# Optimization experiments

Measured on AMD Instinct MI355X. Metric: run time of the kernel, lower is better.

The kernel has to match this reference:

```python
import jax, jax.numpy as jnp
import numpy as np

EMBED_DIM = 128
NUM_EMB = 2048
COMMIT_COST = 0.25
SOFTMAX_COST = 0.0


def setup_inputs() -> dict:
    key = jax.random.key(0)
    k1, k2 = jax.random.split(key)
    z = jax.random.normal(k1, (32, EMBED_DIM, 32, 32), dtype=jnp.float32)
    limit = float(np.sqrt(3.0 / NUM_EMB))  # sonnet-style uniform init
    codebook = jax.random.uniform(k2, (NUM_EMB, EMBED_DIM), minval=-limit, maxval=limit, dtype=jnp.float32)
    return {"z": z, "codebook": codebook}


def _vq_forward(z, codebook):
    B, C, H, W = z.shape  # C == EMBED_DIM (channel_split == 1)
    sg = jax.lax.stop_gradient
    zf = jnp.moveaxis(z, 1, -1).reshape(-1, C)  # [N, d], N = B*H*W
    # squared distances: ||z||^2 + ||e||^2 - 2 z e^T  -> [N, K]
    dist = (jnp.sum(zf * zf, axis=1, keepdims=True)
            + jnp.sum(codebook * codebook, axis=1)
            - 2.0 * (zf @ codebook.T))
    # softmax histogram over spatial positions per batch element: [B, K]
    softmax_hist = jax.nn.softmax(-dist, axis=-1).reshape(B, -1, NUM_EMB).sum(axis=1)
    idx = jnp.argmin(dist, axis=1)  # [N]
    # cross entropy with logits = -dist, target = argmin index
    log_probs = jax.nn.log_softmax(-dist, axis=-1)
    softmax_loss = -jnp.mean(jnp.take_along_axis(log_probs, idx[:, None], axis=1))
    onehot = jax.nn.one_hot(idx, NUM_EMB, dtype=jnp.float32)  # [N, K]
    # index histogram (torch.histc with bins=K,min=0,max=K-1 == integer counts here)
    index_hist = onehot.reshape(B, -1, NUM_EMB).sum(axis=1)  # [B, K]
    zq = (onehot @ codebook).reshape(B, H, W, C)
    zq = jnp.moveaxis(zq, -1, 1)  # [B, C, H, W]
    commitment_loss = jnp.mean((sg(zq) - z) ** 2)
    quantization_loss = jnp.mean((zq - sg(z)) ** 2)
    loss = quantization_loss + COMMIT_COST * commitment_loss + SOFTMAX_COST * softmax_loss
    avg_probs = onehot.mean(axis=0)
    perplexity = jnp.exp(-jnp.sum(avg_probs * jnp.log(avg_probs + 1e-10)))
    onehot_img = jnp.moveaxis(onehot.reshape(B, H, W, NUM_EMB), -1, 1)  # [B, K, H, W]
    idx_img = idx.reshape(B, 1, H, W)
    zq_ste = z + sg(zq - z)  # straight-through estimator
    return (loss, zq_ste, sg(perplexity), onehot_img, idx_img, index_hist,
            softmax_hist, sg(commitment_loss), sg(quantization_loss), sg(softmax_loss))


def reference(z, codebook):
    return _vq_forward(z, codebook)
```

## Files before the change

kernel.cpp:

```cpp
#include <hip/hip_runtime.h>
#include <hip/hip_bf16.h>
#include <float.h>


#define K_NUM 2048
#define D_NUM 128
#define B_NUM 32
#define HW_NUM 1024
#define N_NUM 32768
#define REF_EPS 0.01f

typedef __attribute__((ext_vector_type(8))) short bf16x8;
typedef __attribute__((ext_vector_type(4))) float f32x4;

#define O_LOSS   0ull
#define O_ZQ     1ull
#define O_PERP   4194305ull
#define O_ONEHOT 4194306ull
#define O_IDX    71303170ull
#define O_IHIST  71335938ull
#define O_SHIST  71401474ull
#define O_COMMIT 71467010ull
#define O_QUANT  71467011ull
#define O_SM     71467012ull

#define WS_IDX    0ull
#define WS_SCAL   131072ull
#define WS_EB     131328ull
#define WS_CNORM  1179904ull
#define WS_HIST   1188096ull
#define WS_END    17965312ull

__device__ __noinline__ float vq_exact_dist(const float* zrow, const float* erow,
                                            float zncn) {
    float dot = 0.f;
    for (int c = 0; c < 128; c += 4) {
        float4 zz = *reinterpret_cast<const float4*>(zrow + c);
        float4 ee = *reinterpret_cast<const float4*>(erow + c);
        dot = fmaf(zz.x, -2.f * ee.x, dot);
        dot = fmaf(zz.y, -2.f * ee.y, dot);
        dot = fmaf(zz.z, -2.f * ee.z, dot);
        dot = fmaf(zz.w, -2.f * ee.w, dot);
    }
    return dot + zncn;
}

__global__ void vq_prep(const float* __restrict__ cb, uint* __restrict__ ebuf,
                        float* __restrict__ cnorm) {
    int k = blockIdx.x * 64 + (threadIdx.x >> 2);
    int dc = threadIdx.x & 3;
    float v[32];
    float s = 0.f;
#pragma unroll
    for (int i = 0; i < 8; ++i) {
        float4 x = *reinterpret_cast<const float4*>(cb + (size_t)k * D_NUM + dc * 32 + i * 4);
        v[i * 4 + 0] = x.x; v[i * 4 + 1] = x.y; v[i * 4 + 2] = x.z; v[i * 4 + 3] = x.w;
        s += x.x * x.x + x.y * x.y + x.z * x.z + x.w * x.w;
    }
    s += __shfl_xor(s, 1, 64);
    s += __shfl_xor(s, 2, 64);
    if (dc == 0) cnorm[k] = s;

    int ct = k >> 4, col = k & 15;
    uint4* eb4 = reinterpret_cast<uint4*>(ebuf);
#pragma unroll
    for (int g = 0; g < 4; ++g) {
        uint hw_[4], lw_[4];
#pragma unroll
        for (int t = 0; t < 4; ++t) {
            float x0 = -2.f * v[g * 8 + 2 * t];
            float x1 = -2.f * v[g * 8 + 2 * t + 1];
            uint u0 = __builtin_bit_cast(uint, x0);
            uint u1 = __builtin_bit_cast(uint, x1);
            uint h0 = u0 & 0xffff0000u, h1 = u1 & 0xffff0000u;
            float l0 = x0 - __builtin_bit_cast(float, h0);
            float l1 = x1 - __builtin_bit_cast(float, h1);
            hw_[t] = (h0 >> 16) | h1;
            lw_[t] = (__builtin_bit_cast(uint, l0) >> 16)
                   | (__builtin_bit_cast(uint, l1) & 0xffff0000u);
        }
        int lanedst = (g << 4) | col;
        size_t base = ((size_t)(dc * 128 + ct) * 2) * 64 + lanedst;
        uint4 uh; uh.x = hw_[0]; uh.y = hw_[1]; uh.z = hw_[2]; uh.w = hw_[3];
        uint4 ul; ul.x = lw_[0]; ul.y = lw_[1]; ul.z = lw_[2]; ul.w = lw_[3];
        eb4[base] = uh;
        eb4[base + 64] = ul;
    }
}

template <bool WSH>
__global__ __launch_bounds__(512, 2) void vq_main(
    const float* __restrict__ z, const float* __restrict__ cb,
    const uint* __restrict__ ebuf, const float* __restrict__ cnorm,
    float* __restrict__ out, int* __restrict__ idx_ws, float* __restrict__ scal,
    float* __restrict__ wsh) {
    __shared__ __align__(16) float zt[16][132];
    __shared__ float mredA[8][16];
    __shared__ float mredE[8][16];
    __shared__ int iredE[8][16];
    __shared__ float lred[8][16];

    const int tid = threadIdx.x;
    const int lane = tid & 63;
    const int wv = tid >> 6;
    const int col = lane & 15;
    const int g = lane >> 4;
    const int b = blockIdx.x >> 6;
    const int hw0 = (blockIdx.x & 63) * 16;
    const int n0 = blockIdx.x * 16;

    {
        const float* zb = z + (size_t)b * (D_NUM * HW_NUM) + hw0;
        int d = tid >> 2, q = tid & 3;
        float4 v = *reinterpret_cast<const float4*>(zb + d * HW_NUM + q * 4);
        zt[q * 4 + 0][d] = v.x;
        zt[q * 4 + 1][d] = v.y;
        zt[q * 4 + 2][d] = v.z;
        zt[q * 4 + 3][d] = v.w;
    }
    __syncthreads();

    bf16x8 ah[4], al[4];
#pragma unroll
    for (int dc = 0; dc < 4; ++dc) {
        const float* zr = &zt[col][dc * 32 + g * 8];
        float x[8];
        *reinterpret_cast<float4*>(&x[0]) = *reinterpret_cast<const float4*>(zr);
        *reinterpret_cast<float4*>(&x[4]) = *reinterpret_cast<const float4*>(zr + 4);
        uint hw_[4], lw_[4];
#pragma unroll
        for (int t = 0; t < 4; ++t) {
            uint u0 = __builtin_bit_cast(uint, x[2 * t]);
            uint u1 = __builtin_bit_cast(uint, x[2 * t + 1]);
            uint h0 = u0 & 0xffff0000u, h1 = u1 & 0xffff0000u;
            float l0 = x[2 * t] - __builtin_bit_cast(float, h0);
            float l1 = x[2 * t + 1] - __builtin_bit_cast(float, h1);
            hw_[t] = (h0 >> 16) | h1;
            lw_[t] = (__builtin_bit_cast(uint, l0) >> 16)
                   | (__builtin_bit_cast(uint, l1) & 0xffff0000u);
        }
        uint4 uh; uh.x = hw_[0]; uh.y = hw_[1]; uh.z = hw_[2]; uh.w = hw_[3];
        uint4 ul; ul.x = lw_[0]; ul.y = lw_[1]; ul.z = lw_[2]; ul.w = lw_[3];
        ah[dc] = __builtin_bit_cast(bf16x8, uh);
        al[dc] = __builtin_bit_cast(bf16x8, ul);
    }

    f32x4 acc[16];
#pragma unroll
    for (int ft = 0; ft < 16; ++ft) acc[ft] = (f32x4){0.f, 0.f, 0.f, 0.f};

    const uint4* eb4 = reinterpret_cast<const uint4*>(ebuf);
    const int ctbase = wv << 4;
#pragma unroll
    for (int dc = 0; dc < 4; ++dc) {
#pragma unroll
        for (int ft = 0; ft < 16; ++ft) {
            size_t base = ((size_t)(dc * 128 + ctbase + ft) * 2) * 64 + lane;
            uint4 uh = eb4[base];
            uint4 ul = eb4[base + 64];
            bf16x8 bh = __builtin_bit_cast(bf16x8, uh);
            bf16x8 bl = __builtin_bit_cast(bf16x8, ul);
            acc[ft] = __builtin_amdgcn_mfma_f32_16x16x32_bf16(ah[dc], bh, acc[ft], 0, 0, 0);
            acc[ft] = __builtin_amdgcn_mfma_f32_16x16x32_bf16(al[dc], bh, acc[ft], 0, 0, 0);
            acc[ft] = __builtin_amdgcn_mfma_f32_16x16x32_bf16(ah[dc], bl, acc[ft], 0, 0, 0);
            acc[ft] = __builtin_amdgcn_mfma_f32_16x16x32_bf16(al[dc], bl, acc[ft], 0, 0, 0);
        }
    }

    float zn[4];
    {
        int pz = lane >> 2, part = lane & 3;
        const float* zr = &zt[pz][part * 32];
        float s = 0.f;
#pragma unroll
        for (int i = 0; i < 8; ++i) {
            float4 x = *reinterpret_cast<const float4*>(zr + i * 4);
            s += x.x * x.x + x.y * x.y + x.z * x.z + x.w * x.w;
        }
        s += __shfl_xor(s, 1, 64);
        s += __shfl_xor(s, 2, 64);
#pragma unroll
        for (int r = 0; r < 4; ++r) zn[r] = __shfl(s, (g * 4 + r) * 4, 64);
    }
    float cnv[16];
#pragma unroll
    for (int ft = 0; ft < 16; ++ft) cnv[ft] = cnorm[(wv << 8) + (ft << 4) + col];

#pragma unroll
    for (int ft = 0; ft < 16; ++ft)
#pragma unroll
        for (int r = 0; r < 4; ++r) acc[ft][r] += zn[r] + cnv[ft];

    float mhat[4];
#pragma unroll
    for (int r = 0; r < 4; ++r) {
        float mv = acc[0][r];
#pragma unroll
        for (int ft = 1; ft < 16; ++ft) mv = fminf(mv, acc[ft][r]);
#pragma unroll
        for (int off = 1; off < 16; off <<= 1) mv = fminf(mv, __shfl_xor(mv, off, 64));
        if (col == 0) mredA[wv][g * 4 + r] = mv;
        mhat[r] = mv;
    }
    __syncthreads();
#pragma unroll
    for (int r = 0; r < 4; ++r) {
        int pos = g * 4 + r;
#pragma unroll
        for (int w = 0; w < 8; ++w) mhat[r] = fminf(mhat[r], mredA[w][pos]);
    }

    float cm[4] = {FLT_MAX, FLT_MAX, FLT_MAX, FLT_MAX};
    int ci[4] = {0x7fffffff, 0x7fffffff, 0x7fffffff, 0x7fffffff};
#pragma unroll
    for (int ft = 0; ft < 16; ++ft) {
#pragma unroll
        for (int r = 0; r < 4; ++r) {
            if (acc[ft][r] <= mhat[r] + REF_EPS) {
                int kk = (wv << 8) + (ft << 4) + col;
                float d = vq_exact_dist(&zt[g * 4 + r][0], cb + (size_t)kk * D_NUM,
                                        zn[r] + cnv[ft]);
                if (d < cm[r] || (d == cm[r] && kk < ci[r])) { cm[r] = d; ci[r] = kk; }
            }
        }
    }
    float mstar[4];
    int kstar[4];
#pragma unroll
    for (int r = 0; r < 4; ++r) {
        float mv = cm[r];
        int mi = ci[r];
#pragma unroll
        for (int off = 1; off < 16; off <<= 1) {
            float ov = __shfl_xor(mv, off, 64);
            int oi = __shfl_xor(mi, off, 64);
            if (ov < mv || (ov == mv && oi < mi)) { mv = ov; mi = oi; }
        }
        if (col == 0) { mredE[wv][g * 4 + r] = mv; iredE[wv][g * 4 + r] = mi; }
        mstar[r] = mv;
        kstar[r] = mi;
    }
    __syncthreads();
#pragma unroll
    for (int r = 0; r < 4; ++r) {
        int pos = g * 4 + r;
#pragma unroll
        for (int w = 0; w < 8; ++w) {
            float ov = mredE[w][pos];
            int oi = iredE[w][pos];
            if (ov < mstar[r] || (ov == mstar[r] && oi < kstar[r])) {
                mstar[r] = ov;
                kstar[r] = oi;
            }
        }
    }

#pragma unroll
    for (int r = 0; r < 4; ++r) {
        float s = 0.f;
#pragma unroll
        for (int ft = 0; ft < 16; ++ft) {
            float t = __expf(mhat[r] - acc[ft][r]);
            acc[ft][r] = t;
            s += t;
        }
#pragma unroll
        for (int off = 1; off < 16; off <<= 1) s += __shfl_xor(s, off, 64);
        if (col == 0) lred[wv][g * 4 + r] = s;
    }
    __syncthreads();
    float lf[4], rinv[4];
#pragma unroll
    for (int r = 0; r < 4; ++r) {
        float s = 0.f;
        int pos = g * 4 + r;
#pragma unroll
        for (int w = 0; w < 8; ++w) s += lred[w][pos];
        lf[r] = s;
        rinv[r] = 1.f / s;
    }

#pragma unroll
    for (int ft = 0; ft < 16; ++ft) {
        float h = 0.f;
#pragma unroll
        for (int r = 0; r < 4; ++r) h += acc[ft][r] * rinv[r];
        h += __shfl_xor(h, 16, 64);
        h += __shfl_xor(h, 32, 64);
        if (WSH) {
            if (lane < 16)
                wsh[(size_t)blockIdx.x * K_NUM + (wv << 8) + (ft << 4) + lane] = h;
        } else {
            if (lane < 16)
                atomicAdd(&out[O_SHIST + (size_t)b * K_NUM + (wv << 8) + (ft << 4) + lane], h);
        }
    }

    if (wv == 0) {
        float summ = 0.f, suml = 0.f;
        if (col == 0) {
#pragma unroll
            for (int r = 0; r < 4; ++r) {
                int n = n0 + g * 4 + r;
                idx_ws[n] = kstar[r];
                out[O_IDX + n] = (float)kstar[r];
                atomicAdd(&out[O_IHIST + (size_t)b * K_NUM + kstar[r]], 1.0f);
                summ += mstar[r];
                suml += __logf(lf[r]);
            }
        }
        summ += __shfl_xor(summ, 16, 64);
        summ += __shfl_xor(summ, 32, 64);
        suml += __shfl_xor(suml, 16, 64);
        suml += __shfl_xor(suml, 32, 64);
        if (lane == 0) {
            atomicAdd(&scal[0], summ);
            atomicAdd(&scal[1], suml);
        }
    }
}

__global__ void vq_hist(const float* __restrict__ wsh, float* __restrict__ out) {
    int gid = blockIdx.x * 256 + threadIdx.x;
    int b = gid >> 11;
    int k = gid & 2047;
    const float* p = wsh + ((size_t)b * 64) * K_NUM + k;
    float s = 0.f;
#pragma unroll
    for (int sb = 0; sb < 64; ++sb) s += p[(size_t)sb * K_NUM];
    out[O_SHIST + gid] = s;
}

__global__ void vq_scatter(const int* __restrict__ idx, float* __restrict__ out) {
    int n = blockIdx.x * 256 + threadIdx.x;
    int b = n >> 10;
    int hw = n & 1023;
    int k = idx[n];
    out[O_ONEHOT + (((size_t)b * K_NUM + k) << 10) + hw] = 1.0f;
}

__global__ void vq_zq(const int* __restrict__ idx,
                      const float* __restrict__ cb, float* __restrict__ out) {
    __shared__ int sidx[64];
    __shared__ float lcb[64][129];
    int t = threadIdx.x;
    int b = blockIdx.x >> 4;
    int hw0 = (blockIdx.x & 15) * 64;
    if (t < 64) sidx[t] = idx[b * HW_NUM + hw0 + t];
    __syncthreads();
    for (int i = t; i < 2048; i += 256) {
        int row = i >> 5;
        int col = (i & 31) * 4;
        float4 v = *reinterpret_cast<const float4*>(cb + (size_t)sidx[row] * D_NUM + col);
        lcb[row][col + 0] = v.x;
        lcb[row][col + 1] = v.y;
        lcb[row][col + 2] = v.z;
        lcb[row][col + 3] = v.w;
    }
    __syncthreads();
    int hwl = t & 63;
    int c0 = t >> 6;
#pragma unroll
    for (int cc = 0; cc < 32; ++cc) {
        int c = cc * 4 + c0;
        out[O_ZQ + (((size_t)b * D_NUM + c) << 10) + hw0 + hwl] = lcb[hwl][c];
    }
}

__global__ void vq_finalize(float* __restrict__ out, const float* __restrict__ scal) {
    __shared__ float red[256];
    int t = threadIdx.x;
    float ent = 0.f;
    for (int k = t; k < K_NUM; k += 256) {
        float c = 0.f;
#pragma unroll
        for (int b = 0; b < B_NUM; ++b) c += out[O_IHIST + (size_t)b * K_NUM + k];
        float p = c * (1.f / 32768.f);
        ent += p * __logf(p + 1e-10f);
    }
    red[t] = ent;
    __syncthreads();
    for (int s = 128; s; s >>= 1) {
        if (t < s) red[t] += red[t + s];
        __syncthreads();
    }
    if (t == 0) {
        float mse = scal[0] * (1.f / (32768.f * 128.f));
        out[O_LOSS] = 1.25f * mse;
        out[O_PERP] = __expf(-red[0]);
        out[O_COMMIT] = mse;
        out[O_QUANT] = mse;
        out[O_SM] = scal[1] * (1.f / 32768.f);
    }
}

extern "C" void kernel_launch(void* const* d_in, const int* in_sizes, int n_in,
                              void* d_out, int out_size, void* d_ws, size_t ws_size,
                              hipStream_t stream) {
    const float* z = (const float*)d_in[0];
    const float* cb = (const float*)d_in[1];
    float* out = (float*)d_out;
    char* ws = (char*)d_ws;

    int* idx_ws = (int*)(ws + WS_IDX);
    float* scal = (float*)(ws + WS_SCAL);
    uint* ebuf = (uint*)(ws + WS_EB);
    float* cnorm = (float*)(ws + WS_CNORM);
    float* wsh = (float*)(ws + WS_HIST);
    const bool big = ws_size >= WS_END;

    hipMemsetAsync(scal, 0, 2 * sizeof(float), stream);
    hipMemsetAsync(out + O_IHIST, 0, 2 * B_NUM * K_NUM * sizeof(float), stream);
    hipMemsetAsync(out + O_ONEHOT, 0, (size_t)B_NUM * K_NUM * HW_NUM * sizeof(float),
                   stream);

    vq_prep<<<32, 256, 0, stream>>>(cb, ebuf, cnorm);
    if (big)
        vq_main<true><<<2048, 512, 0, stream>>>(z, cb, ebuf, cnorm, out, idx_ws, scal, wsh);
    else
        vq_main<false><<<2048, 512, 0, stream>>>(z, cb, ebuf, cnorm, out, idx_ws, scal, wsh);
    vq_scatter<<<128, 256, 0, stream>>>(idx_ws, out);
    vq_zq<<<512, 256, 0, stream>>>(idx_ws, cb, out);
    if (big) vq_hist<<<256, 256, 0, stream>>>(wsh, out);
    vq_finalize<<<1, 256, 0, stream>>>(out, scal);
}
```

Baseline: 595.0 us.

## Prefetch codebook tiles, drop lo*lo MFMA term, fuse one-hot zero-fill with scatter

The main distance kernel now software-pipelines the codebook fragment loads through a four-slot register ring, so global loads are issued ahead of the MFMAs that consume them. The z hi/lo split is now computed per d-chunk instead of all at once. The low*low bf16 correction product is dropped, which cuts MFMA work by a quarter at a small cost in distance precision that could flip near-tie argmins. The full-buffer memset followed by a sparse scatter is replaced with one dense kernel that writes 0/1 for every one-hot element, so the large output is written once instead of zeroed and then patched.

Result: no change. 590.1 us (-0.8%).

```diff
diff --git a/kernel.cpp b/kernel.cpp
--- a/kernel.cpp
+++ b/kernel.cpp
@@ -120,52 +120,61 @@
     }
     __syncthreads();
 
-    bf16x8 ah[4], al[4];
-#pragma unroll
-    for (int dc = 0; dc < 4; ++dc) {
-        const float* zr = &zt[col][dc * 32 + g * 8];
-        float x[8];
-        *reinterpret_cast<float4*>(&x[0]) = *reinterpret_cast<const float4*>(zr);
-        *reinterpret_cast<float4*>(&x[4]) = *reinterpret_cast<const float4*>(zr + 4);
-        uint hw_[4], lw_[4];
-#pragma unroll
-        for (int t = 0; t < 4; ++t) {
-            uint u0 = __builtin_bit_cast(uint, x[2 * t]);
-            uint u1 = __builtin_bit_cast(uint, x[2 * t + 1]);
-            uint h0 = u0 & 0xffff0000u, h1 = u1 & 0xffff0000u;
-            float l0 = x[2 * t] - __builtin_bit_cast(float, h0);
-            float l1 = x[2 * t + 1] - __builtin_bit_cast(float, h1);
-            hw_[t] = (h0 >> 16) | h1;
-            lw_[t] = (__builtin_bit_cast(uint, l0) >> 16)
-                   | (__builtin_bit_cast(uint, l1) & 0xffff0000u);
-        }
-        uint4 uh; uh.x = hw_[0]; uh.y = hw_[1]; uh.z = hw_[2]; uh.w = hw_[3];
-        uint4 ul; ul.x = lw_[0]; ul.y = lw_[1]; ul.z = lw_[2]; ul.w = lw_[3];
-        ah[dc] = __builtin_bit_cast(bf16x8, uh);
-        al[dc] = __builtin_bit_cast(bf16x8, ul);
-    }
-
     f32x4 acc[16];
 #pragma unroll
     for (int ft = 0; ft < 16; ++ft) acc[ft] = (f32x4){0.f, 0.f, 0.f, 0.f};
 
     const uint4* eb4 = reinterpret_cast<const uint4*>(ebuf);
     const int ctbase = wv << 4;
+
+    uint4 su[4], sv[4];
+#define LOADP(slot, DC, FT)                                                    \
+    {                                                                          \
+        size_t base_ = ((size_t)((DC) * 128 + ctbase + (FT)) * 2) * 64 + lane; \
+        su[slot] = eb4[base_];                                                 \
+        sv[slot] = eb4[base_ + 64];                                            \
+    }
+
+    LOADP(0, 0, 0) LOADP(1, 0, 1) LOADP(2, 0, 2) LOADP(3, 0, 3)
+
 #pragma unroll
     for (int dc = 0; dc < 4; ++dc) {
+        bf16x8 ahc, alc;
+        {
+            const float* zr = &zt[col][dc * 32 + g * 8];
+            float x[8];
+            *reinterpret_cast<float4*>(&x[0]) = *reinterpret_cast<const float4*>(zr);
+            *reinterpret_cast<float4*>(&x[4]) = *reinterpret_cast<const float4*>(zr + 4);
+            uint hw_[4], lw_[4];
+#pragma unroll
+            for (int t = 0; t < 4; ++t) {
+                uint u0 = __builtin_bit_cast(uint, x[2 * t]);
+                uint u1 = __builtin_bit_cast(uint, x[2 * t + 1]);
+                uint h0 = u0 & 0xffff0000u, h1 = u1 & 0xffff0000u;
+                float l0 = x[2 * t] - __builtin_bit_cast(float, h0);
+                float l1 = x[2 * t + 1] - __builtin_bit_cast(float, h1);
+                hw_[t] = (h0 >> 16) | h1;
+                lw_[t] = (__builtin_bit_cast(uint, l0) >> 16)
+                       | (__builtin_bit_cast(uint, l1) & 0xffff0000u);
+            }
+            uint4 uh; uh.x = hw_[0]; uh.y = hw_[1]; uh.z = hw_[2]; uh.w = hw_[3];
+            uint4 ul; ul.x = lw_[0]; ul.y = lw_[1]; ul.z = lw_[2]; ul.w = lw_[3];
+            ahc = __builtin_bit_cast(bf16x8, uh);
+            alc = __builtin_bit_cast(bf16x8, ul);
+        }
 #pragma unroll
         for (int ft = 0; ft < 16; ++ft) {
-            size_t base = ((size_t)(dc * 128 + ctbase + ft) * 2) * 64 + lane;
-            uint4 uh = eb4[base];
-            uint4 ul = eb4[base + 64];
-            bf16x8 bh = __builtin_bit_cast(bf16x8, uh);
-            bf16x8 bl = __builtin_bit_cast(bf16x8, ul);
-            acc[ft] = __builtin_amdgcn_mfma_f32_16x16x32_bf16(ah[dc], bh, acc[ft], 0, 0, 0);
-            acc[ft] = __builtin_amdgcn_mfma_f32_16x16x32_bf16(al[dc], bh, acc[ft], 0, 0, 0);
-            acc[ft] = __builtin_amdgcn_mfma_f32_16x16x32_bf16(ah[dc], bl, acc[ft], 0, 0, 0);
-            acc[ft] = __builtin_amdgcn_mfma_f32_16x16x32_bf16(al[dc], bl, acc[ft], 0, 0, 0);
-        }
-    }
+            const int slot = ft & 3;
+            bf16x8 bh = __builtin_bit_cast(bf16x8, su[slot]);
+            bf16x8 bl = __builtin_bit_cast(bf16x8, sv[slot]);
+            acc[ft] = __builtin_amdgcn_mfma_f32_16x16x32_bf16(ahc, bh, acc[ft], 0, 0, 0);
+            acc[ft] = __builtin_amdgcn_mfma_f32_16x16x32_bf16(alc, bh, acc[ft], 0, 0, 0);
+            acc[ft] = __builtin_amdgcn_mfma_f32_16x16x32_bf16(ahc, bl, acc[ft], 0, 0, 0);
+            const int tn = dc * 16 + ft + 4;
+            if (tn < 64) { LOADP(slot, (tn >> 4), (tn & 15)) }
+        }
+    }
+#undef LOADP
 
     float zn[4];
     {
@@ -331,12 +340,17 @@
     out[O_SHIST + gid] = s;
 }
 
-__global__ void vq_scatter(const int* __restrict__ idx, float* __restrict__ out) {
-    int n = blockIdx.x * 256 + threadIdx.x;
-    int b = n >> 10;
-    int hw = n & 1023;
-    int k = idx[n];
-    out[O_ONEHOT + (((size_t)b * K_NUM + k) << 10) + hw] = 1.0f;
+__global__ void vq_onehot(const int* __restrict__ idx, float* __restrict__ out) {
+    size_t gid = (size_t)blockIdx.x * 256 + threadIdx.x;
+    size_t i = gid * 4;
+    int hw = (int)(i & 1023);
+    int k = (int)((i >> 10) & 2047);
+    int b = (int)(i >> 21);
+    int4 iv = *reinterpret_cast<const int4*>(idx + b * HW_NUM + hw);
+    float2 v0 = {iv.x == k ? 1.f : 0.f, iv.y == k ? 1.f : 0.f};
+    float2 v1 = {iv.z == k ? 1.f : 0.f, iv.w == k ? 1.f : 0.f};
+    *reinterpret_cast<float2*>(out + O_ONEHOT + i) = v0;
+    *reinterpret_cast<float2*>(out + O_ONEHOT + i + 2) = v1;
 }
 
 __global__ void vq_zq(const int* __restrict__ idx,
@@ -411,15 +425,13 @@
 
     hipMemsetAsync(scal, 0, 2 * sizeof(float), stream);
     hipMemsetAsync(out + O_IHIST, 0, 2 * B_NUM * K_NUM * sizeof(float), stream);
-    hipMemsetAsync(out + O_ONEHOT, 0, (size_t)B_NUM * K_NUM * HW_NUM * sizeof(float),
-                   stream);
 
     vq_prep<<<32, 256, 0, stream>>>(cb, ebuf, cnorm);
     if (big)
         vq_main<true><<<2048, 512, 0, stream>>>(z, cb, ebuf, cnorm, out, idx_ws, scal, wsh);
     else
         vq_main<false><<<2048, 512, 0, stream>>>(z, cb, ebuf, cnorm, out, idx_ws, scal, wsh);
-    vq_scatter<<<128, 256, 0, stream>>>(idx_ws, out);
+    vq_onehot<<<65536, 256, 0, stream>>>(idx_ws, out);
     vq_zq<<<512, 256, 0, stream>>>(idx_ws, cb, out);
     if (big) vq_hist<<<256, 256, 0, stream>>>(wsh, out);
     vq_finalize<<<1, 256, 0, stream>>>(out, scal);
```
